# Kernel optimization log

Hardware: AMD Instinct MI355X
Metric: run time of the kernel (lower is better)

Reference implementation:

```python
import jax, jax.numpy as jnp
import numpy as np

B, S, H, NH, D = 2, 2048, 2048, 16, 128
SCALE = D ** -0.5


def _rotate_half(x):
    x1, x2 = jnp.split(x, 2, axis=-1)
    return jnp.concatenate([-x2, x1], axis=-1)


def setup_inputs() -> dict:
    key = jax.random.key(0)
    ks = jax.random.split(key, 6)
    hidden_states = jax.random.normal(ks[0], (B, S, H), dtype=jnp.float32)
    # causal additive mask (batch, 1, q_len, kv_len)
    causal = jnp.where(jnp.tril(jnp.ones((S, S), dtype=bool)), 0.0, -1e9).astype(jnp.float32)
    attention_mask = jnp.broadcast_to(causal[None, None], (B, 1, S, S))
    # standard RoPE tables, theta=10000
    inv_freq = 1.0 / (10000.0 ** (jnp.arange(0, D, 2, dtype=jnp.float32) / D))
    t = jnp.arange(S, dtype=jnp.float32)
    freqs = jnp.einsum('s,f->sf', t, inv_freq)
    emb = jnp.concatenate([freqs, freqs], axis=-1)  # (S, D)
    rope_cos = jnp.cos(emb)[None, None]  # (1,1,S,D)
    rope_sin = jnp.sin(emb)[None, None]
    w_std = H ** -0.5
    Wq = jax.random.normal(ks[1], (H, NH * D), dtype=jnp.float32) * w_std
    Wk = jax.random.normal(ks[2], (H, D), dtype=jnp.float32) * w_std
    Wv = jax.random.normal(ks[3], (H, D), dtype=jnp.float32) * w_std
    Wo = jax.random.normal(ks[4], (NH * D, H), dtype=jnp.float32) * ((NH * D) ** -0.5)
    return {
        'hidden_states': hidden_states,
        'attention_mask': attention_mask,
        'rope_cos': rope_cos,
        'rope_sin': rope_sin,
        'Wq': Wq, 'Wk': Wk, 'Wv': Wv, 'Wo': Wo,
    }


def reference(hidden_states, attention_mask, rope_cos, rope_sin, Wq, Wk, Wv, Wo):
    b, s, _ = hidden_states.shape
    q = (hidden_states @ Wq).reshape(b, s, NH, D).transpose(0, 2, 1, 3)  # (b,h,s,d)
    k = (hidden_states @ Wk)[:, None]  # (b,1,s,d) single shared KV head
    v = (hidden_states @ Wv)[:, None]
    # inline RoPE on q and the shared k
    q = q * rope_cos + _rotate_half(q) * rope_sin
    k = k * rope_cos + _rotate_half(k) * rope_sin
    k = k[:, 0]  # (b,s,d); broadcast over heads instead of expand
    v = v[:, 0]
    scores = jnp.einsum('bhqd,bkd->bhqk', q, k) * SCALE + attention_mask
    attn = jax.nn.softmax(scores.astype(jnp.float32), axis=-1).astype(q.dtype)
    out = jnp.einsum('bhqk,bkd->bhqd', attn, v)
    out = out.transpose(0, 2, 1, 3).reshape(b, s, NH * D)
    return out @ Wo
```

## Files before the change

### kernel.cpp

```cpp
#include <hip/hip_runtime.h>
#include <hip/hip_bf16.h>

#define NB 2
#define NS 2048
#define NHID 2048
#define NHEAD 16
#define ND 128
#define NM (NB*NS)

typedef __attribute__((ext_vector_type(8))) short s16x8;
typedef __attribute__((ext_vector_type(4))) float f32x4;
typedef unsigned long long ull;

__device__ __forceinline__ short f2bf(float x) {
  unsigned u = __float_as_uint(x);
  u = (u + 0x7fffu + ((u >> 16) & 1u)) >> 16;
  return (short)u;
}

__device__ __forceinline__ int colmap(int wc, int ni) {
  return (ni < 2) ? (wc*32 + ni*16) : (64 + wc*32 + (ni-2)*16);
}

__device__ __forceinline__ void gload16(const short* g, short* l) {
  __builtin_amdgcn_global_load_lds(
      (const __attribute__((address_space(1))) void*)g,
      (__attribute__((address_space(3))) void*)l, 16, 0, 0);
}

__global__ __launch_bounds__(256) void cvt_f32_bf16(const float* __restrict__ src,
                                                    short* __restrict__ dst, int n4) {
  int i = blockIdx.x*256 + threadIdx.x;
  if (i >= n4) return;
  const float4 v = reinterpret_cast<const float4*>(src)[i];
  ull pk =
      (ull)(unsigned short)f2bf(v.x)
    | ((ull)(unsigned short)f2bf(v.y) << 16)
    | ((ull)(unsigned short)f2bf(v.z) << 32)
    | ((ull)(unsigned short)f2bf(v.w) << 48);
  reinterpret_cast<ull*>(dst)[i] = pk;
}

__global__ __launch_bounds__(256) void cvtT(const float* __restrict__ src,
                                            short* __restrict__ dst, int K, int N) {
  __shared__ float t[32][33];
  const int n0 = blockIdx.x*32, k0 = blockIdx.y*32;
  const int tx = threadIdx.x & 31, ty = threadIdx.x >> 5;
  #pragma unroll
  for (int i = 0; i < 4; ++i)
    t[ty + 8*i][tx] = src[(size_t)(k0 + ty + 8*i)*N + n0 + tx];
  __syncthreads();
  #pragma unroll
  for (int i = 0; i < 4; ++i)
    dst[(size_t)(n0 + ty + 8*i)*K + k0 + tx] = f2bf(t[tx][ty + 8*i]);
}

__global__ __launch_bounds__(256) void trans_v(const short* __restrict__ src,
                                               short* __restrict__ dst) {
  __shared__ short t[32][40];
  const int c0 = blockIdx.x*32;
  const int r0 = blockIdx.y*32;
  const int tx = threadIdx.x & 31, ty = threadIdx.x >> 5;
  #pragma unroll
  for (int i = 0; i < 4; ++i)
    t[ty + 8*i][tx] = src[(size_t)(r0 + ty + 8*i)*128 + c0 + tx];
  __syncthreads();
  #pragma unroll
  for (int i = 0; i < 4; ++i) {
    const int d = c0 + ty + 8*i;
    dst[(size_t)d*4096 + ((r0 + tx) ^ ((d & 7) << 3))] = t[tx][ty + 8*i];
  }
}

__global__ __launch_bounds__(256) void gemm_qkv(
    const short* __restrict__ hsb, const short* __restrict__ WqT,
    const short* __restrict__ WkT, const short* __restrict__ WvT,
    const float* __restrict__ ropeC, const float* __restrict__ ropeS,
    short* __restrict__ Qb, short* __restrict__ Kb, short* __restrict__ Vb)
{
  const int tid = threadIdx.x;
  const int lane = tid & 63, wid = tid >> 6;
  const int wr = wid >> 1, wc = wid & 1;
  const int l15 = lane & 15, l4 = lane >> 4;
  const int m0 = blockIdx.x * 128;
  const int ny = blockIdx.y;
  const short* Bt = (ny < 16) ? (WqT + (size_t)ny*128*2048) : (ny == 16 ? WkT : WvT);

  __shared__ short Al[128][32];
  __shared__ short Bl[128][32];

  f32x4 acc[4][4];
  const f32x4 zf = {0.f,0.f,0.f,0.f};
  #pragma unroll
  for (int i=0;i<4;++i)
    #pragma unroll
    for (int j=0;j<4;++j) acc[i][j] = zf;

  const int srow = tid >> 2;
  const int scol = (tid & 3) * 8;
  const short* Ap0 = hsb + (size_t)(m0 + srow)*2048 + scol;
  const short* Ap1 = hsb + (size_t)(m0 + 64 + srow)*2048 + scol;
  const short* Bp0 = Bt + (size_t)srow*2048 + scol;
  const short* Bp1 = Bt + (size_t)(64 + srow)*2048 + scol;
  short* AL0 = &Al[0][0] + tid*8;
  short* AL1 = &Al[0][0] + 2048 + tid*8;
  short* BL0 = &Bl[0][0] + tid*8;
  short* BL1 = &Bl[0][0] + 2048 + tid*8;

  for (int kt = 0; kt < 64; ++kt) {
    const int k0 = kt * 32;
    __syncthreads();
    gload16(Ap0 + k0, AL0);
    gload16(Ap1 + k0, AL1);
    gload16(Bp0 + k0, BL0);
    gload16(Bp1 + k0, BL1);
    __syncthreads();
    s16x8 af[4], bfr[4];
    #pragma unroll
    for (int mi=0; mi<4; ++mi) af[mi] = *(const s16x8*)&Al[wr*64 + mi*16 + l15][l4*8];
    #pragma unroll
    for (int ni=0; ni<4; ++ni) bfr[ni] = *(const s16x8*)&Bl[colmap(wc,ni) + l15][l4*8];
    #pragma unroll
    for (int mi=0; mi<4; ++mi)
      #pragma unroll
      for (int ni=0; ni<4; ++ni)
        acc[mi][ni] = __builtin_amdgcn_mfma_f32_16x16x32_bf16(af[mi], bfr[ni], acc[mi][ni], 0,0,0);
  }

  const bool isQ = (ny < 16), isK = (ny == 16);
  #pragma unroll
  for (int mi=0; mi<4; ++mi) {
    #pragma unroll
    for (int r=0; r<4; ++r) {
      const int mrow = m0 + wr*64 + mi*16 + l4*4 + r;
      const int s = mrow & 2047;
      const int bb = mrow >> 11;
      if (!isQ && !isK) {
        #pragma unroll
        for (int ni=0; ni<4; ++ni) {
          const int d = colmap(wc,ni) + l15;
          Vb[(size_t)mrow*128 + d] = f2bf(acc[mi][ni][r]);
        }
      } else {
        #pragma unroll
        for (int ni=0; ni<2; ++ni) {
          const int d = colmap(wc,ni) + l15;
          const float c0 = ropeC[s*128 + d],      s0 = ropeS[s*128 + d];
          const float c1 = ropeC[s*128 + d + 64], s1 = ropeS[s*128 + d + 64];
          const float x0 = acc[mi][ni][r], x1 = acc[mi][ni+2][r];
          const float y0 = x0*c0 - x1*s0;
          const float y1 = x1*c1 + x0*s1;
          if (isK) {
            const int dsw = d ^ ((s & 7) << 3);
            Kb[(size_t)mrow*128 + dsw]      = f2bf(y0);
            Kb[(size_t)mrow*128 + dsw + 64] = f2bf(y1);
          } else {
            const size_t base = ((size_t)(bb*16 + ny)*2048 + s)*128;
            Qb[base + d]      = f2bf(y0);
            Qb[base + d + 64] = f2bf(y1);
          }
        }
      }
    }
  }
}

__device__ __forceinline__ void qkt_pair(const short* KL, const s16x8 (&qfH)[4],
                                         const s16x8 (&qfL)[4], f32x4 (&scH)[4],
                                         f32x4 (&scL)[4], int l15, int l4, int sw) {
  __builtin_amdgcn_s_setprio(1);
  #pragma unroll
  for (int kk=0; kk<4; ++kk)
    #pragma unroll
    for (int n=0; n<4; ++n) {
      s16x8 kf = *(const s16x8*)&KL[(n*16 + l15)*128 + ((kk*32 + l4*8) ^ sw)];
      scH[n] = __builtin_amdgcn_mfma_f32_16x16x32_bf16(kf, qfH[kk], scH[n], 0,0,0);
      scL[n] = __builtin_amdgcn_mfma_f32_16x16x32_bf16(kf, qfL[kk], scL[n], 0,0,0);
    }
  __builtin_amdgcn_s_setprio(0);
}

__device__ __forceinline__ void qkt_one(const short* KL, const s16x8 (&qf)[4],
                                        f32x4 (&sc)[4], int l15, int l4, int sw) {
  __builtin_amdgcn_s_setprio(1);
  #pragma unroll
  for (int kk=0; kk<4; ++kk)
    #pragma unroll
    for (int n=0; n<4; ++n) {
      s16x8 kf = *(const s16x8*)&KL[(n*16 + l15)*128 + ((kk*32 + l4*8) ^ sw)];
      sc[n] = __builtin_amdgcn_mfma_f32_16x16x32_bf16(kf, qf[kk], sc[n], 0,0,0);
    }
  __builtin_amdgcn_s_setprio(0);
}

__device__ __forceinline__ void sm16(f32x4 (&sc)[4], bool diag, int wid, int l15, int l4,
                                     int sw, float &m_run, float &l_run, f32x4 (&o)[8],
                                     short* Pl) {
  const float CEXP = 0.08838834764831845f * 1.44269504088896340f;
  float p[4][4];
  #pragma unroll
  for (int n=0;n<4;++n)
    #pragma unroll
    for (int r=0;r<4;++r) {
      float sv = sc[n][r];
      if (diag && (n*16 + l4*4 + r > wid*16 + l15)) sv = -1e30f;
      p[n][r] = sv;
    }
  float pm = p[0][0];
  #pragma unroll
  for (int n=0;n<4;++n)
    #pragma unroll
    for (int r=0;r<4;++r) pm = fmaxf(pm, p[n][r]);
  pm = fmaxf(pm, __shfl_xor(pm, 16));
  pm = fmaxf(pm, __shfl_xor(pm, 32));
  const float mn = fmaxf(m_run, pm);
  const float al = exp2f((m_run - mn) * CEXP);
  m_run = mn;
  float rs = 0.f;
  #pragma unroll
  for (int n=0;n<4;++n)
    #pragma unroll
    for (int r=0;r<4;++r) { p[n][r] = exp2f((p[n][r] - mn) * CEXP); rs += p[n][r]; }
  rs += __shfl_xor(rs, 16);
  rs += __shfl_xor(rs, 32);
  l_run = l_run * al + rs;
  #pragma unroll
  for (int r=0;r<4;++r) {
    const float a = __shfl(al, l4*4 + r);
    #pragma unroll
    for (int i=0;i<8;++i) o[i][r] *= a;
  }
  #pragma unroll
  for (int n=0;n<4;++n) {
    ull w =
        (ull)(unsigned short)f2bf(p[n][0])
      | ((ull)(unsigned short)f2bf(p[n][1]) << 16)
      | ((ull)(unsigned short)f2bf(p[n][2]) << 32)
      | ((ull)(unsigned short)f2bf(p[n][3]) << 48);
    *(ull*)&Pl[l15*64 + ((n*16 + l4*4) ^ sw)] = w;
  }
}

__device__ __forceinline__ void pv_pair(const short* VL, const s16x8 (&paH)[2],
                                        const s16x8 (&paL)[2], f32x4 (&oH)[8],
                                        f32x4 (&oL)[8], int l15, int l4, int sw) {
  __builtin_amdgcn_s_setprio(1);
  #pragma unroll
  for (int kb=0; kb<2; ++kb)
    #pragma unroll
    for (int d8=0; d8<8; ++d8) {
      s16x8 vf = *(const s16x8*)&VL[(d8*16 + l15)*64 + ((kb*32 + l4*8) ^ sw)];
      oH[d8] = __builtin_amdgcn_mfma_f32_16x16x32_bf16(paH[kb], vf, oH[d8], 0,0,0);
      oL[d8] = __builtin_amdgcn_mfma_f32_16x16x32_bf16(paL[kb], vf, oL[d8], 0,0,0);
    }
  __builtin_amdgcn_s_setprio(0);
}

__device__ __forceinline__ void pv_one(const short* VL, const s16x8 (&pa)[2],
                                       f32x4 (&o)[8], int l15, int l4, int sw) {
  __builtin_amdgcn_s_setprio(1);
  #pragma unroll
  for (int kb=0; kb<2; ++kb)
    #pragma unroll
    for (int d8=0; d8<8; ++d8) {
      s16x8 vf = *(const s16x8*)&VL[(d8*16 + l15)*64 + ((kb*32 + l4*8) ^ sw)];
      o[d8] = __builtin_amdgcn_mfma_f32_16x16x32_bf16(pa[kb], vf, o[d8], 0,0,0);
    }
  __builtin_amdgcn_s_setprio(0);
}

__global__ __launch_bounds__(256) void attn_fwd(
    const short* __restrict__ Qb, const short* __restrict__ Kb,
    const short* __restrict__ VbT, short* __restrict__ Ob)
{
  const int tid = threadIdx.x;
  const int lane = tid & 63, wid = tid >> 6;
  const int l15 = lane & 15, l4 = lane >> 4;
  const int bid = blockIdx.x;
  const int wg = (bid & 7)*64 + (bid >> 3);
  const int pr = wg & 15, h = (wg >> 4) & 15, b = wg >> 8;
  const int lo = pr, hi = 31 - pr;
  const int sw = (l15 & 7) << 3;

  __shared__ short Kl[2][64*128];
  __shared__ short Vt[2][128*64];
  __shared__ short Pb[4][2][16*64];
  short* PlH = &Pb[wid][0][0];
  short* PlL = &Pb[wid][1][0];

  s16x8 qfH[4], qfL[4];
  {
    const short* QpL = Qb + ((size_t)(b*16 + h)*2048 + lo*64 + wid*16 + l15)*128 + l4*8;
    const short* QpH = Qb + ((size_t)(b*16 + h)*2048 + hi*64 + wid*16 + l15)*128 + l4*8;
    #pragma unroll
    for (int kk=0; kk<4; ++kk) { qfL[kk] = *(const s16x8*)(QpL + kk*32);
                                 qfH[kk] = *(const s16x8*)(QpH + kk*32); }
  }

  float mH = -1e30f, lH = 0.f, mL = -1e30f, lL = 0.f;
  f32x4 oH[8], oL[8];
  const f32x4 zf = {0.f,0.f,0.f,0.f};
  #pragma unroll
  for (int i=0;i<8;++i){ oH[i]=zf; oL[i]=zf; }

  const short* Kg = Kb + (size_t)b*2048*128;
  const short* Vg = VbT + (size_t)b*2048;

  #define STAGE(bufi, tt) do {                                              \
    const int kv0_ = (tt)*64;                                               \
    _Pragma("unroll")                                                       \
    for (int rep=0; rep<4; ++rep) {                                         \
      const int c = tid + rep*256;                                          \
      gload16(Kg + (size_t)(kv0_ + (c>>4))*128 + (c&15)*8, &Kl[bufi][c*8]); \
    }                                                                       \
    _Pragma("unroll")                                                       \
    for (int rep=0; rep<4; ++rep) {                                         \
      const int c = tid + rep*256;                                          \
      gload16(Vg + (size_t)(c>>3)*4096 + kv0_ + (c&7)*8, &Vt[bufi][c*8]);   \
    }                                                                       \
  } while(0)

  STAGE(0, 0);
  __syncthreads();
  int buf = 0;
  int t = 0;

  for (; t <= lo; ++t) {
    STAGE(buf^1, t+1);
    const short* KL = &Kl[buf][0];
    const short* VL = &Vt[buf][0];
    f32x4 scH[4], scL[4];
    #pragma unroll
    for (int n=0;n<4;++n){ scH[n]=zf; scL[n]=zf; }
    qkt_pair(KL, qfH, qfL, scH, scL, l15, l4, sw);
    sm16(scH, false, wid, l15, l4, sw, mH, lH, oH, PlH);
    sm16(scL, (t == lo), wid, l15, l4, sw, mL, lL, oL, PlL);
    s16x8 paH[2], paL[2];
    #pragma unroll
    for (int kb=0; kb<2; ++kb) {
      paH[kb] = *(const s16x8*)&PlH[l15*64 + ((kb*32 + l4*8) ^ sw)];
      paL[kb] = *(const s16x8*)&PlL[l15*64 + ((kb*32 + l4*8) ^ sw)];
    }
    pv_pair(VL, paH, paL, oH, oL, l15, l4, sw);
    __syncthreads();
    buf ^= 1;
  }
  for (; t <= hi; ++t) {
    if (t < hi) STAGE(buf^1, t+1);
    const short* KL = &Kl[buf][0];
    const short* VL = &Vt[buf][0];
    f32x4 scH[4];
    #pragma unroll
    for (int n=0;n<4;++n) scH[n]=zf;
    qkt_one(KL, qfH, scH, l15, l4, sw);
    sm16(scH, (t == hi), wid, l15, l4, sw, mH, lH, oH, PlH);
    s16x8 paH[2];
    #pragma unroll
    for (int kb=0; kb<2; ++kb)
      paH[kb] = *(const s16x8*)&PlH[l15*64 + ((kb*32 + l4*8) ^ sw)];
    pv_one(VL, paH, oH, l15, l4, sw);
    __syncthreads();
    buf ^= 1;
  }
  #undef STAGE

  const float invH = 1.0f / lH;
  const float invL = 1.0f / lL;
  #pragma unroll
  for (int r=0;r<4;++r) {
    const float iH = __shfl(invH, l4*4 + r);
    const float iL = __shfl(invL, l4*4 + r);
    const size_t baseH = ((size_t)(b*2048) + hi*64 + wid*16 + l4*4 + r)*2048 + (size_t)h*128;
    const size_t baseL = ((size_t)(b*2048) + lo*64 + wid*16 + l4*4 + r)*2048 + (size_t)h*128;
    #pragma unroll
    for (int d8=0; d8<8; ++d8) {
      Ob[baseH + d8*16 + l15] = f2bf(oH[d8][r] * iH);
      Ob[baseL + d8*16 + l15] = f2bf(oL[d8][r] * iL);
    }
  }
}

__global__ __launch_bounds__(256) void gemm_out(
    const short* __restrict__ Ob, const short* __restrict__ WoT,
    float* __restrict__ out)
{
  const int tid = threadIdx.x;
  const int lane = tid & 63, wid = tid >> 6;
  const int wr = wid >> 1, wc = wid & 1;
  const int l15 = lane & 15, l4 = lane >> 4;
  const int m0 = blockIdx.x * 128;
  const int n0 = blockIdx.y * 128;

  __shared__ short Al[128][32];
  __shared__ short Bl[128][32];

  f32x4 acc[4][4];
  const f32x4 zf = {0.f,0.f,0.f,0.f};
  #pragma unroll
  for (int i=0;i<4;++i)
    #pragma unroll
    for (int j=0;j<4;++j) acc[i][j] = zf;

  const int srow = tid >> 2;
  const int scol = (tid & 3) * 8;
  const short* Ap0 = Ob + (size_t)(m0 + srow)*2048 + scol;
  const short* Ap1 = Ob + (size_t)(m0 + 64 + srow)*2048 + scol;
  const short* Bp0 = WoT + (size_t)(n0 + srow)*2048 + scol;
  const short* Bp1 = WoT + (size_t)(n0 + 64 + srow)*2048 + scol;
  short* AL0 = &Al[0][0] + tid*8;
  short* AL1 = &Al[0][0] + 2048 + tid*8;
  short* BL0 = &Bl[0][0] + tid*8;
  short* BL1 = &Bl[0][0] + 2048 + tid*8;

  for (int kt = 0; kt < 64; ++kt) {
    const int k0 = kt * 32;
    __syncthreads();
    gload16(Ap0 + k0, AL0);
    gload16(Ap1 + k0, AL1);
    gload16(Bp0 + k0, BL0);
    gload16(Bp1 + k0, BL1);
    __syncthreads();
    s16x8 af[4], bfr[4];
    #pragma unroll
    for (int mi=0; mi<4; ++mi) af[mi] = *(const s16x8*)&Al[wr*64 + mi*16 + l15][l4*8];
    #pragma unroll
    for (int ni=0; ni<4; ++ni) bfr[ni] = *(const s16x8*)&Bl[colmap(wc,ni) + l15][l4*8];
    #pragma unroll
    for (int mi=0; mi<4; ++mi)
      #pragma unroll
      for (int ni=0; ni<4; ++ni)
        acc[mi][ni] = __builtin_amdgcn_mfma_f32_16x16x32_bf16(af[mi], bfr[ni], acc[mi][ni], 0,0,0);
  }

  #pragma unroll
  for (int mi=0; mi<4; ++mi)
    #pragma unroll
    for (int r=0; r<4; ++r) {
      const int mrow = m0 + wr*64 + mi*16 + l4*4 + r;
      #pragma unroll
      for (int ni=0; ni<4; ++ni)
        out[(size_t)mrow*2048 + n0 + colmap(wc,ni) + l15] = acc[mi][ni][r];
    }
}

extern "C" void kernel_launch(void* const* d_in, const int* in_sizes, int n_in,
                              void* d_out, int out_size, void* d_ws, size_t ws_size,
                              hipStream_t stream) {
  const float* hidden = (const float*)d_in[0];
  const float* ropeC  = (const float*)d_in[2];
  const float* ropeS  = (const float*)d_in[3];
  const float* Wq     = (const float*)d_in[4];
  const float* Wk     = (const float*)d_in[5];
  const float* Wv     = (const float*)d_in[6];
  const float* Wo     = (const float*)d_in[7];
  float* out = (float*)d_out;
  char* ws = (char*)d_ws;

  short* hsb = (short*)(ws + 0);
  short* WqT = (short*)(ws + 16777216);
  short* WkT = (short*)(ws + 25165824);
  short* WvT = (short*)(ws + 25690112);
  short* WoT = (short*)(ws + 26214400);
  short* Qb  = (short*)(ws + 34603008);
  short* Kb  = (short*)(ws + 51380224);
  short* Vb  = (short*)(ws + 52428800);
  short* VbT = (short*)(ws + 53477376);
  short* Ob  = hsb;

  cvt_f32_bf16<<<dim3((NM*NHID/4 + 255)/256), dim3(256), 0, stream>>>(hidden, hsb, NM*NHID/4);
  cvtT<<<dim3(64,64), dim3(256), 0, stream>>>(Wq, WqT, 2048, 2048);
  cvtT<<<dim3(4, 64), dim3(256), 0, stream>>>(Wk, WkT, 2048, 128);
  cvtT<<<dim3(4, 64), dim3(256), 0, stream>>>(Wv, WvT, 2048, 128);
  cvtT<<<dim3(64,64), dim3(256), 0, stream>>>(Wo, WoT, 2048, 2048);

  gemm_qkv<<<dim3(NM/128, 18), dim3(256), 0, stream>>>(hsb, WqT, WkT, WvT, ropeC, ropeS, Qb, Kb, Vb);
  trans_v<<<dim3(4, 128), dim3(256), 0, stream>>>(Vb, VbT);
  attn_fwd<<<dim3(512), dim3(256), 0, stream>>>(Qb, Kb, VbT, Ob);
  gemm_out<<<dim3(NM/128, 2048/128), dim3(256), 0, stream>>>(Ob, WoT, out);
}
```

Baseline: 412.0 us.

## Add hardware exp/bf16-pack intrinsics, lazy softmax rescale, and XCD-aware GEMM block remap

Swaps the software bf16 rounding for the v_cvt_pk_bf16_f32 instruction and exp2f for a raw v_exp_f32, both in the conversion kernel and in the attention softmax. The online softmax now skips rescaling the output accumulators unless the block max rises more than a threshold above the running max, and it folds the subtract-and-scale into a single fma. Both GEMMs go from 2D grids to flattened 1D grids whose block IDs are remapped so tiles are spread across the 8 XCDs for better L2 locality. The lazy rescale can let exponentials exceed 1 by up to 2^(8*scale), and the raw exp has slightly looser accuracy.

```diff
diff --git a/kernel.cpp b/kernel.cpp
--- a/kernel.cpp
+++ b/kernel.cpp
@@ -18,6 +18,13 @@
   return (short)u;
 }
 
+__device__ __forceinline__ float fexp2(float x) {
+  float r; asm("v_exp_f32 %0, %1" : "=v"(r) : "v"(x)); return r;
+}
+__device__ __forceinline__ unsigned cvtpk(float lo, float hi) {
+  unsigned r; asm("v_cvt_pk_bf16_f32 %0, %1, %2" : "=v"(r) : "v"(lo), "v"(hi)); return r;
+}
+
 __device__ __forceinline__ int colmap(int wc, int ni) {
   return (ni < 2) ? (wc*32 + ni*16) : (64 + wc*32 + (ni-2)*16);
 }
@@ -34,10 +41,8 @@
   if (i >= n4) return;
   const float4 v = reinterpret_cast<const float4*>(src)[i];
   ull pk =
-      (ull)(unsigned short)f2bf(v.x)
-    | ((ull)(unsigned short)f2bf(v.y) << 16)
-    | ((ull)(unsigned short)f2bf(v.z) << 32)
-    | ((ull)(unsigned short)f2bf(v.w) << 48);
+      (ull)(unsigned)cvtpk(v.x, v.y)
+    | ((ull)(unsigned)cvtpk(v.z, v.w) << 32);
   reinterpret_cast<ull*>(dst)[i] = pk;
 }
 
@@ -82,8 +87,10 @@
   const int lane = tid & 63, wid = tid >> 6;
   const int wr = wid >> 1, wc = wid & 1;
   const int l15 = lane & 15, l4 = lane >> 4;
-  const int m0 = blockIdx.x * 128;
-  const int ny = blockIdx.y;
+  const int bid = blockIdx.x;
+  const int wg = (bid & 7) * 72 + (bid >> 3);
+  const int m0 = (wg & 31) * 128;
+  const int ny = wg >> 5;
   const short* Bt = (ny < 16) ? (WqT + (size_t)ny*128*2048) : (ny == 16 ? WkT : WvT);
 
   __shared__ short Al[128][32];
@@ -201,44 +208,57 @@
   #pragma unroll
   for (int n=0;n<4;++n)
     #pragma unroll
-    for (int r=0;r<4;++r) {
-      float sv = sc[n][r];
-      if (diag && (n*16 + l4*4 + r > wid*16 + l15)) sv = -1e30f;
-      p[n][r] = sv;
-    }
-  float pm = p[0][0];
-  #pragma unroll
-  for (int n=0;n<4;++n)
-    #pragma unroll
-    for (int r=0;r<4;++r) pm = fmaxf(pm, p[n][r]);
+    for (int r=0;r<4;++r) p[n][r] = sc[n][r];
+  if (diag) {
+    #pragma unroll
+    for (int n=0;n<4;++n)
+      #pragma unroll
+      for (int r=0;r<4;++r)
+        if (n*16 + l4*4 + r > wid*16 + l15) p[n][r] = -1e30f;
+  }
+  float a0 = fmaxf(fmaxf(p[0][0], p[0][1]), p[0][2]);
+  float a1 = fmaxf(fmaxf(p[0][3], p[1][0]), p[1][1]);
+  float a2 = fmaxf(fmaxf(p[1][2], p[1][3]), p[2][0]);
+  float a3 = fmaxf(fmaxf(p[2][1], p[2][2]), p[2][3]);
+  float a4 = fmaxf(fmaxf(p[3][0], p[3][1]), p[3][2]);
+  float b0 = fmaxf(fmaxf(a0, a1), a2);
+  float b1 = fmaxf(fmaxf(a3, a4), p[3][3]);
+  float pm = fmaxf(b0, b1);
   pm = fmaxf(pm, __shfl_xor(pm, 16));
   pm = fmaxf(pm, __shfl_xor(pm, 32));
-  const float mn = fmaxf(m_run, pm);
-  const float al = exp2f((m_run - mn) * CEXP);
-  m_run = mn;
+
+  if (!__all(pm <= m_run + 8.0f)) {
+    const float mn = fmaxf(m_run, pm);
+    const float al = fexp2((m_run - mn) * CEXP);
+    m_run = mn;
+    l_run *= al;
+    #pragma unroll
+    for (int r=0;r<4;++r) {
+      const float a = __shfl(al, l4*4 + r);
+      #pragma unroll
+      for (int i=0;i<8;++i) o[i][r] *= a;
+    }
+  }
+  const float mC = m_run * CEXP;
+  #pragma unroll
+  for (int n=0;n<4;++n)
+    #pragma unroll
+    for (int r=0;r<4;++r)
+      p[n][r] = fexp2(__builtin_fmaf(p[n][r], CEXP, -mC));
+  #pragma unroll
+  for (int n=0;n<4;++n) {
+    ull w = (ull)(unsigned)cvtpk(p[n][0], p[n][1])
+          | ((ull)(unsigned)cvtpk(p[n][2], p[n][3]) << 32);
+    *(ull*)&Pl[l15*64 + ((n*16 + l4*4) ^ sw)] = w;
+  }
   float rs = 0.f;
   #pragma unroll
   for (int n=0;n<4;++n)
     #pragma unroll
-    for (int r=0;r<4;++r) { p[n][r] = exp2f((p[n][r] - mn) * CEXP); rs += p[n][r]; }
+    for (int r=0;r<4;++r) rs += p[n][r];
   rs += __shfl_xor(rs, 16);
   rs += __shfl_xor(rs, 32);
-  l_run = l_run * al + rs;
-  #pragma unroll
-  for (int r=0;r<4;++r) {
-    const float a = __shfl(al, l4*4 + r);
-    #pragma unroll
-    for (int i=0;i<8;++i) o[i][r] *= a;
-  }
-  #pragma unroll
-  for (int n=0;n<4;++n) {
-    ull w =
-        (ull)(unsigned short)f2bf(p[n][0])
-      | ((ull)(unsigned short)f2bf(p[n][1]) << 16)
-      | ((ull)(unsigned short)f2bf(p[n][2]) << 32)
-      | ((ull)(unsigned short)f2bf(p[n][3]) << 48);
-    *(ull*)&Pl[l15*64 + ((n*16 + l4*4) ^ sw)] = w;
-  }
+  l_run += rs;
 }
 
 __device__ __forceinline__ void pv_pair(const short* VL, const s16x8 (&paH)[2],
@@ -388,8 +408,10 @@
   const int lane = tid & 63, wid = tid >> 6;
   const int wr = wid >> 1, wc = wid & 1;
   const int l15 = lane & 15, l4 = lane >> 4;
-  const int m0 = blockIdx.x * 128;
-  const int n0 = blockIdx.y * 128;
+  const int bid = blockIdx.x;
+  const int wg = (bid & 7) * 64 + (bid >> 3);
+  const int m0 = (wg & 31) * 128;
+  const int n0 = (wg >> 5) * 128;
 
   __shared__ short Al[128][32];
   __shared__ short Bl[128][32];
@@ -473,8 +495,8 @@
   cvtT<<<dim3(4, 64), dim3(256), 0, stream>>>(Wv, WvT, 2048, 128);
   cvtT<<<dim3(64,64), dim3(256), 0, stream>>>(Wo, WoT, 2048, 2048);
 
-  gemm_qkv<<<dim3(NM/128, 18), dim3(256), 0, stream>>>(hsb, WqT, WkT, WvT, ropeC, ropeS, Qb, Kb, Vb);
+  gemm_qkv<<<dim3(576), dim3(256), 0, stream>>>(hsb, WqT, WkT, WvT, ropeC, ropeS, Qb, Kb, Vb);
   trans_v<<<dim3(4, 128), dim3(256), 0, stream>>>(Vb, VbT);
   attn_fwd<<<dim3(512), dim3(256), 0, stream>>>(Qb, Kb, VbT, Ob);
-  gemm_out<<<dim3(NM/128, 2048/128), dim3(256), 0, stream>>>(Ob, WoT, out);
-}
+  gemm_out<<<dim3(512), dim3(256), 0, stream>>>(Ob, WoT, out);
+}
```

After: 410.0 us. Within noise of the previous version (-0.5%).
